# Kernel optimization log

Measured on AMD Instinct MI355X. Metric: run time of the kernel, lower is better.

Reference implementation:

```python
import jax, jax.numpy as jnp
import numpy as np

N = 8192
IN_DIM = 512
OUT_DIM = 512


def setup_inputs() -> dict:
    key = jax.random.key(0)
    kA, kX, k1, k2, k3, k4 = jax.random.split(key, 6)
    A = jax.random.uniform(kA, (N, N), dtype=jnp.float32)  # strictly positive -> nonzero triu
    X = jax.random.normal(kX, (N, IN_DIM), dtype=jnp.float32)
    s = 1.0 / np.sqrt(IN_DIM)
    W1 = jax.random.uniform(k1, (OUT_DIM, IN_DIM), minval=-s, maxval=s, dtype=jnp.float32)  # fc
    b1 = jax.random.uniform(k2, (OUT_DIM,), minval=-s, maxval=s, dtype=jnp.float32)
    W2 = jax.random.uniform(k3, (OUT_DIM, IN_DIM), minval=-s, maxval=s, dtype=jnp.float32)  # fc2
    b2 = jax.random.uniform(k4, (OUT_DIM,), minval=-s, maxval=s, dtype=jnp.float32)
    return {"A": A, "X": X, "W1": W1, "b1": b1, "W2": W2, "b2": b2}


def reference(A, X, W1, b1, W2, b2):
    n = A.shape[0]
    # strictly upper-triangular mask (diagonal=1); with uniform(0,1) fill all these
    # entries are nonzero, so torch.nonzero selects exactly them: m = n(n-1)/2 values.
    triu_mask = jnp.triu(jnp.ones((n, n), dtype=bool), k=1)
    m = n * (n - 1) // 2
    # torch.median = lower median = sorted[(m-1)//2]; pad non-triu entries with +inf
    vals = jnp.where(triu_mask, A, jnp.inf).reshape(-1)
    median_value = jnp.sort(vals)[(m - 1) // 2]
    # A[A < median] = 0
    A_thr = jnp.where(A < median_value, jnp.zeros((), A.dtype), A)
    A_norm = jax.nn.softmax(A_thr, axis=-1)
    fcX = X @ W1.T + b1    # [N, out_dim]
    fc2X = X @ W2.T + b2   # [N, out_dim]
    out = jax.nn.leaky_relu(0.1 * fc2X + 0.9 * (A_norm @ fcX), negative_slope=0.01)
    return out
```

## Files before the change

### kernel.cpp

```cpp
#include <hip/hip_runtime.h>

#define DEVI __device__ __forceinline__

typedef __attribute__((ext_vector_type(8))) short short8;
typedef __attribute__((ext_vector_type(4))) float f32x4;

static constexpr int NN = 8192;
static constexpr int DD = 512;
static constexpr unsigned LOB = 0x3EFE0000u;
static constexpr unsigned HIB = 0x3F020000u;
static constexpr long long K_RANK = 16775167LL;

static constexpr size_t WS_HIST = 0;
static constexpr size_t WS_CNT  = 1048576;
static constexpr size_t WS_MED  = 1048832;
static constexpr size_t WS_XB   = 2097152;
static constexpr size_t WS_W1B  = WS_XB  + (size_t)NN * DD * 2;
static constexpr size_t WS_W2B  = WS_W1B + (size_t)DD * DD * 2;
static constexpr size_t WS_FCXT = WS_W2B + (size_t)DD * DD * 2;
static constexpr size_t WS_FC2  = WS_FCXT + (size_t)NN * DD * 2;
static constexpr size_t WS_UP   = WS_FC2 + (size_t)NN * DD * 4;
static constexpr size_t WS_ZP   = WS_UP  + (size_t)4 * NN * DD * 2;

DEVI unsigned short f2bf(float f) {
  unsigned u = __float_as_uint(f);
  u += 0x7fffu + ((u >> 16) & 1u);
  return (unsigned short)(u >> 16);
}
DEVI float bf2f(unsigned short h) { return __uint_as_float(((unsigned)h) << 16); }
DEVI int swz(int row, int kq) { return kq ^ ((row >> 1) & 3); }

DEVI void gl_lds16(const void* g, void* l) {
  __builtin_amdgcn_global_load_lds(
      (const __attribute__((address_space(1))) unsigned*)g,
      (__attribute__((address_space(3))) unsigned*)l, 16, 0, 0);
}

#define VMCNT(n) asm volatile("s_waitcnt vmcnt(" #n ")" ::: "memory")
#define LGKM0 asm volatile("s_waitcnt lgkmcnt(0)" ::: "memory")

__global__ __launch_bounds__(256) void hist_k(const float* __restrict__ A,
                                              unsigned* __restrict__ hist,
                                              unsigned* __restrict__ below) {
  unsigned cnt = 0;
  const long long nt = (long long)gridDim.x * blockDim.x;
  const float4* A4 = (const float4*)A;
  for (long long q = (long long)blockIdx.x * blockDim.x + threadIdx.x; q < 16777216LL; q += nt) {
    long long base = q << 2;
    int row = (int)(base >> 13);
    int col = (int)(base & 8191);
    if (col + 3 <= row) continue;
    float4 v = A4[q];
    float vv[4] = {v.x, v.y, v.z, v.w};
#pragma unroll
    for (int j = 0; j < 4; ++j) {
      if (col + j > row) {
        unsigned u = __float_as_uint(vv[j]);
        if (u < LOB) cnt++;
        else if (u < HIB) atomicAdd(&hist[u - LOB], 1u);
      }
    }
  }
  for (int off = 32; off > 0; off >>= 1) cnt += __shfl_down(cnt, off);
  if ((threadIdx.x & 63) == 0 && cnt) atomicAdd(below, cnt);
}

__global__ __launch_bounds__(1024) void select_k(const unsigned* __restrict__ hist,
                                                 const unsigned* __restrict__ below,
                                                 unsigned* __restrict__ med) {
  __shared__ unsigned ssum[1024];
  __shared__ int owner;
  __shared__ unsigned tg_s;
  const int t = threadIdx.x;
  unsigned own = 0;
#pragma unroll 4
  for (int b = 0; b < 256; ++b) own += hist[t * 256 + b];
  ssum[t] = own;
  __syncthreads();
  for (int off = 1; off < 1024; off <<= 1) {
    unsigned v = (t >= off) ? ssum[t - off] : 0u;
    __syncthreads();
    ssum[t] += v;
    __syncthreads();
  }
  long long target = K_RANK - (long long)(*below);
  unsigned incl = ssum[t];
  unsigned excl = incl - own;
  if (target >= (long long)excl && target < (long long)incl) {
    owner = t;
    tg_s = (unsigned)(target - (long long)excl);
  }
  __syncthreads();
  const int to = owner;
  const unsigned tg = tg_s;
  unsigned v256 = (t < 256) ? hist[to * 256 + t] : 0u;
  __syncthreads();
  if (t < 256) ssum[t] = v256;
  __syncthreads();
  for (int off = 1; off < 256; off <<= 1) {
    unsigned v = (t < 256 && t >= off) ? ssum[t - off] : 0u;
    __syncthreads();
    if (t < 256) ssum[t] += v;
    __syncthreads();
  }
  if (t < 256) {
    unsigned incl2 = ssum[t];
    unsigned excl2 = incl2 - v256;
    if (tg >= excl2 && tg < incl2) *med = LOB + (unsigned)(to * 256 + t);
  }
}

__global__ __launch_bounds__(256) void convert_k(const float* __restrict__ X,
                                                 const float* __restrict__ W1,
                                                 const float* __restrict__ W2,
                                                 unsigned short* __restrict__ Xb,
                                                 unsigned short* __restrict__ W1b,
                                                 unsigned short* __restrict__ W2b) {
  const long long nt = (long long)gridDim.x * blockDim.x;
  const long long NX = (long long)NN * DD;
  const long long NW = (long long)DD * DD;
  for (long long q = (long long)blockIdx.x * blockDim.x + threadIdx.x; q < (NX + 2 * NW) / 4; q += nt) {
    long long e = q << 2;
    const float4* src; unsigned short* dst; long long off;
    if (e < NX)            { src = (const float4*)X;  dst = Xb;  off = e; }
    else if (e < NX + NW)  { src = (const float4*)W1; dst = W1b; off = e - NX; }
    else                   { src = (const float4*)W2; dst = W2b; off = e - NX - NW; }
    float4 v = src[off >> 2];
    ushort4 o;
    o.x = f2bf(v.x); o.y = f2bf(v.y); o.z = f2bf(v.z); o.w = f2bf(v.w);
    *(ushort4*)(dst + off) = o;
  }
}

template <bool BROW, bool OBF>
__global__ __launch_bounds__(512, 2) void gemm_small_k(const unsigned short* __restrict__ Am,
                                                       const unsigned short* __restrict__ Bm,
                                                       const float* __restrict__ bias,
                                                       void* __restrict__ outp, int ldout) {
  __shared__ alignas(16) unsigned short Ap[64 * 32];
  __shared__ alignas(16) unsigned short Bt[256 * 32];
  char* apB = (char*)Ap;
  char* btB = (char*)Bt;
  const int tid = threadIdx.x, lane = tid & 63, w = tid >> 6;
  const int wm = w >> 2, wn = w & 3;
  const int lr = lane & 15, lq = lane >> 4;
  const int m0 = blockIdx.y * 64, n0 = blockIdx.x * 256;
  const int rL = lane >> 2, kq = lane & 3;
  f32x4 acc[2][4];
#pragma unroll
  for (int i = 0; i < 2; ++i)
#pragma unroll
    for (int j = 0; j < 4; ++j) acc[i][j] = (f32x4){0.f, 0.f, 0.f, 0.f};

#pragma unroll 1
  for (int kt = 0; kt < 16; ++kt) {
    const int k0 = kt * 32;
    __syncthreads();
    if (w < 4) {
      int r = w * 16 + rL;
      gl_lds16(Am + ((size_t)(m0 + r) * DD + k0 + swz(r, kq) * 8), apB + w * 1024);
    }
#pragma unroll
    for (int i = 0; i < 2; ++i) {
      int blk = w * 2 + i;
      int r = blk * 16 + rL;
      gl_lds16(Bm + ((size_t)(n0 + r) * DD + k0 + swz(r, kq) * 8), btB + blk * 1024);
    }
    __syncthreads();
    short8 a[2], b[4];
#pragma unroll
    for (int fr = 0; fr < 2; ++fr) {
      int r = wm * 32 + fr * 16 + lr;
      a[fr] = *(const short8*)(apB + r * 64 + swz(r, lq) * 16);
    }
#pragma unroll
    for (int fc = 0; fc < 4; ++fc) {
      int r = wn * 64 + fc * 16 + lr;
      b[fc] = *(const short8*)(btB + r * 64 + swz(r, lq) * 16);
    }
#pragma unroll
    for (int fr = 0; fr < 2; ++fr)
#pragma unroll
      for (int fc = 0; fc < 4; ++fc)
        acc[fr][fc] = __builtin_amdgcn_mfma_f32_16x16x32_bf16(a[fr], b[fc], acc[fr][fc], 0, 0, 0);
  }
#pragma unroll
  for (int fr = 0; fr < 2; ++fr)
#pragma unroll
    for (int fc = 0; fc < 4; ++fc)
#pragma unroll
      for (int j = 0; j < 4; ++j) {
        int row = m0 + wm * 32 + fr * 16 + lq * 4 + j;
        int col = n0 + wn * 64 + fc * 16 + lr;
        float v = acc[fr][fc][j] + (BROW ? bias[row] : bias[col]);
        if (OBF) ((unsigned short*)outp)[(size_t)row * ldout + col] = f2bf(v);
        else     ((float*)outp)[(size_t)row * ldout + col] = v;
      }
}

static constexpr int LDS_A0 = 0;
static constexpr int LDS_A1 = 8192;
static constexpr int LDS_B0 = 16384;
static constexpr int LDS_B1 = 49152;

__global__ __launch_bounds__(512, 2) void main_gemm_k(const float* __restrict__ A,
                                                      const unsigned short* __restrict__ fcXT,
                                                      const unsigned* __restrict__ medp,
                                                      unsigned short* __restrict__ Up,
                                                      float* __restrict__ Zp) {
  __shared__ alignas(16) char lds[81920];
  const int tid = threadIdx.x, lane = tid & 63, w = tid >> 6;
  const int wm = w >> 2, wn = w & 3;
  const int lr = lane & 15, lq = lane >> 4;
  const int ks = blockIdx.x;
  const int m0 = blockIdx.y * 128;
  const int kbase = ks * 2048;
  const float med = __uint_as_float(*medp);
  const int rB = lane >> 2, kqB = lane & 3;
  const int rA = tid >> 2, cqA = tid & 3;
  const float* aRow = A + (size_t)(m0 + rA) * NN;
  const int ldsAw = rA * 64 + swz(rA, cqA) * 16;

  float zacc = 0.f;
  f32x4 acc[4][8];
#pragma unroll
  for (int i = 0; i < 4; ++i)
#pragma unroll
    for (int j = 0; j < 8; ++j) acc[i][j] = (f32x4){0.f, 0.f, 0.f, 0.f};
  float4 vA00, vA01, vA10, vA11;

#define CONV8(V0, V1, DST)                                                     \
  {                                                                            \
    float vv[8] = {V0.x, V0.y, V0.z, V0.w, V1.x, V1.y, V1.z, V1.w};            \
    short8 pb;                                                                 \
    _Pragma("unroll")                                                          \
    for (int j = 0; j < 8; ++j) {                                              \
      float a_ = vv[j];                                                        \
      float p_ = (a_ < med) ? 1.0f : __expf(a_);                               \
      unsigned short h_ = f2bf(p_);                                            \
      pb[j] = (short)h_;                                                       \
      zacc += bf2f(h_);                                                        \
    }                                                                          \
    *(short8*)(DST) = pb;                                                      \
  }

  {
#pragma unroll
    for (int i = 0; i < 4; ++i) {
      int blk = w * 4 + i;
      int o = blk * 16 + rB;
      gl_lds16(fcXT + ((size_t)o * NN + kbase + swz(o, kqB) * 8), lds + LDS_B0 + blk * 1024);
    }
    const float* ap0 = aRow + kbase + cqA * 8;
    float4 t0 = *(const float4*)ap0;
    float4 t1 = *(const float4*)(ap0 + 4);
    vA00 = *(const float4*)(ap0 + 32);
    vA01 = *(const float4*)(ap0 + 36);
    CONV8(t0, t1, lds + LDS_A0 + ldsAw);
  }
  __syncthreads();

#define ITER(KT, CUR, NCUR, VAC0, VAC1, VAN0, VAN1)                            \
  {                                                                            \
    const int kt_ = (KT);                                                      \
    if (kt_ < 63) {                                                            \
      const int k1 = kbase + (kt_ + 1) * 32;                                   \
      _Pragma("unroll")                                                        \
      for (int i = 0; i < 4; ++i) {                                            \
        int blk = w * 4 + i;                                                   \
        int o = blk * 16 + rB;                                                 \
        gl_lds16(fcXT + ((size_t)o * NN + k1 + swz(o, kqB) * 8),               \
                 lds + LDS_B##NCUR + blk * 1024);                              \
      }                                                                        \
      if (kt_ < 62) {                                                          \
        const float* apf = aRow + kbase + (kt_ + 2) * 32 + cqA * 8;            \
        asm volatile("global_load_dwordx4 %0, %2, off\n\t"                     \
                     "global_load_dwordx4 %1, %2, off offset:16"               \
                     : "=&v"(VAN0), "=&v"(VAN1)                                \
                     : "v"(apf)                                                \
                     : "memory");                                              \
      }                                                                        \
    }                                                                          \
    short8 af[4], bfr[8];                                                      \
    _Pragma("unroll")                                                          \
    for (int fr = 0; fr < 4; ++fr) {                                           \
      int r = wm * 64 + fr * 16 + lr;                                          \
      af[fr] = *(const short8*)(lds + LDS_A##CUR + r * 64 + swz(r, lq) * 16);  \
    }                                                                          \
    _Pragma("unroll")                                                          \
    for (int fc = 0; fc < 8; ++fc) {                                           \
      int o = wn * 128 + fc * 16 + lr;                                         \
      bfr[fc] = *(const short8*)(lds + LDS_B##CUR + o * 64 + swz(o, lq) * 16); \
    }                                                                          \
    __builtin_amdgcn_s_setprio(1);                                             \
    _Pragma("unroll")                                                          \
    for (int fr = 0; fr < 4; ++fr)                                             \
      _Pragma("unroll")                                                        \
      for (int fc = 0; fc < 8; ++fc)                                           \
        acc[fr][fc] = __builtin_amdgcn_mfma_f32_16x16x32_bf16(af[fr], bfr[fc], \
                                                              acc[fr][fc], 0, 0, 0); \
    __builtin_amdgcn_s_setprio(0);                                             \
    if (kt_ < 63) {                                                            \
      if (kt_ < 62) { VMCNT(6); } else { VMCNT(4); }                           \
      __builtin_amdgcn_sched_barrier(0);                                       \
      CONV8(VAC0, VAC1, lds + LDS_A##NCUR + ldsAw);                            \
      if (kt_ < 62) { VMCNT(2); } else { VMCNT(0); }                           \
      LGKM0;                                                                   \
      __builtin_amdgcn_s_barrier();                                            \
    }                                                                          \
  }

#pragma unroll 1
  for (int t2 = 0; t2 < 32; ++t2) {
    ITER(2 * t2,     0, 1, vA00, vA01, vA10, vA11);
    ITER(2 * t2 + 1, 1, 0, vA10, vA11, vA00, vA01);
  }
#undef ITER
#undef CONV8

  zacc += __shfl_xor(zacc, 1);
  zacc += __shfl_xor(zacc, 2);
  if ((lane & 3) == 0) Zp[(size_t)ks * NN + m0 + rA] = zacc;
#pragma unroll
  for (int fr = 0; fr < 4; ++fr)
#pragma unroll
    for (int fc = 0; fc < 8; ++fc)
#pragma unroll
      for (int j = 0; j < 4; ++j) {
        int row = m0 + wm * 64 + fr * 16 + lq * 4 + j;
        int col = wn * 128 + fc * 16 + lr;
        Up[((size_t)ks << 22) + ((size_t)row << 9) + col] = f2bf(acc[fr][fc][j]);
      }
}

__global__ __launch_bounds__(256) void reduce_k(const unsigned short* __restrict__ Up,
                                                const float* __restrict__ Zp,
                                                const float* __restrict__ fc2,
                                                float* __restrict__ out) {
  long long t = (long long)blockIdx.x * blockDim.x + threadIdx.x;
  if (t >= (long long)NN * DD / 8) return;
  long long base = t << 3;
  int row = (int)(base >> 9);
  float Z = Zp[row] + Zp[NN + row] + Zp[2 * NN + row] + Zp[3 * NN + row];
  float inv = 0.9f / Z;
  float s[8] = {0, 0, 0, 0, 0, 0, 0, 0};
#pragma unroll
  for (int sp = 0; sp < 4; ++sp) {
    const uint4 u = *(const uint4*)(Up + ((long long)sp << 22) + base);
    const unsigned uu[4] = {u.x, u.y, u.z, u.w};
#pragma unroll
    for (int j = 0; j < 4; ++j) {
      s[2 * j]     += __uint_as_float(uu[j] << 16);
      s[2 * j + 1] += __uint_as_float(uu[j] & 0xffff0000u);
    }
  }
  float4 fa = *(const float4*)(fc2 + base);
  float4 fb = *(const float4*)(fc2 + base + 4);
  float fv[8] = {fa.x, fa.y, fa.z, fa.w, fb.x, fb.y, fb.z, fb.w};
  float o[8];
#pragma unroll
  for (int j = 0; j < 8; ++j) {
    float v = 0.1f * fv[j] + inv * s[j];
    o[j] = v >= 0.f ? v : 0.01f * v;
  }
  *(float4*)(out + base)     = (float4){o[0], o[1], o[2], o[3]};
  *(float4*)(out + base + 4) = (float4){o[4], o[5], o[6], o[7]};
}

extern "C" void kernel_launch(void* const* d_in, const int* in_sizes, int n_in,
                              void* d_out, int out_size, void* d_ws, size_t ws_size,
                              hipStream_t stream) {
  const float* A  = (const float*)d_in[0];
  const float* X  = (const float*)d_in[1];
  const float* W1 = (const float*)d_in[2];
  const float* b1 = (const float*)d_in[3];
  const float* W2 = (const float*)d_in[4];
  const float* b2 = (const float*)d_in[5];
  char* ws = (char*)d_ws;
  unsigned* hist = (unsigned*)(ws + WS_HIST);
  unsigned* cnt  = (unsigned*)(ws + WS_CNT);
  unsigned* med  = (unsigned*)(ws + WS_MED);
  unsigned short* Xb   = (unsigned short*)(ws + WS_XB);
  unsigned short* W1b  = (unsigned short*)(ws + WS_W1B);
  unsigned short* W2b  = (unsigned short*)(ws + WS_W2B);
  unsigned short* fcXT = (unsigned short*)(ws + WS_FCXT);
  float* fc2           = (float*)(ws + WS_FC2);
  unsigned short* Upp  = (unsigned short*)(ws + WS_UP);
  float* Zp            = (float*)(ws + WS_ZP);

  hipMemsetAsync(ws, 0, 1048576 + 512, stream);
  hipLaunchKernelGGL(hist_k, dim3(2048), dim3(256), 0, stream, A, hist, cnt);
  hipLaunchKernelGGL(select_k, dim3(1), dim3(1024), 0, stream, hist, cnt, med);
  hipLaunchKernelGGL(convert_k, dim3(1024), dim3(256), 0, stream, X, W1, W2, Xb, W1b, W2b);
  hipLaunchKernelGGL((gemm_small_k<true, true>), dim3(32, 8), dim3(512), 0, stream,
                     W1b, Xb, b1, (void*)fcXT, NN);
  hipLaunchKernelGGL((gemm_small_k<false, false>), dim3(2, 128), dim3(512), 0, stream,
                     Xb, W2b, b2, (void*)fc2, DD);
  hipLaunchKernelGGL(main_gemm_k, dim3(4, 64), dim3(512), 0, stream, A, fcXT, med, Upp, Zp);
  hipLaunchKernelGGL(reduce_k, dim3(2048), dim3(256), 0, stream, Upp, Zp, fc2, (float*)d_out);
}
```

Before: 293.6 us.

## Merge hist/convert and both small GEMMs into combined launches, remap grid for XCD locality

Combines the histogram pass and the bf16 conversion into one kernel that splits its blocks by role. It also merges the two small GEMMs into one launch and vectorises the histogram prefix read in select_k. The main GEMM grid becomes 1D, with a block-id mapping that keeps each K-split on a pair of XCDs so those blocks share A rows and fcXT in the same L2. The aim is to cut launch gaps and tail idling between small kernels and to improve cache locality. The cost is role-branching blocks with uneven work in each fused launch.

```diff
diff --git a/kernel.cpp b/kernel.cpp
--- a/kernel.cpp
+++ b/kernel.cpp
@@ -39,13 +39,32 @@
 #define VMCNT(n) asm volatile("s_waitcnt vmcnt(" #n ")" ::: "memory")
 #define LGKM0 asm volatile("s_waitcnt lgkmcnt(0)" ::: "memory")
 
-__global__ __launch_bounds__(256) void hist_k(const float* __restrict__ A,
-                                              unsigned* __restrict__ hist,
-                                              unsigned* __restrict__ below) {
+
+DEVI void convert_body(const float* __restrict__ X, const float* __restrict__ W1,
+                       const float* __restrict__ W2, unsigned short* __restrict__ Xb,
+                       unsigned short* __restrict__ W1b, unsigned short* __restrict__ W2b,
+                       int cb, int tid) {
+  const long long NX = (long long)NN * DD;
+  const long long NW = (long long)DD * DD;
+  const long long total4 = (NX + 2 * NW) / 4;
+  for (long long q = (long long)cb * 512 + tid; q < total4; q += 65536LL) {
+    long long e = q << 2;
+    const float4* src; unsigned short* dst; long long off;
+    if (e < NX)           { src = (const float4*)X;  dst = Xb;  off = e; }
+    else if (e < NX + NW) { src = (const float4*)W1; dst = W1b; off = e - NX; }
+    else                  { src = (const float4*)W2; dst = W2b; off = e - NX - NW; }
+    float4 v = src[off >> 2];
+    ushort4 o;
+    o.x = f2bf(v.x); o.y = f2bf(v.y); o.z = f2bf(v.z); o.w = f2bf(v.w);
+    *(ushort4*)(dst + off) = o;
+  }
+}
+
+DEVI void hist_body(const float* __restrict__ A, unsigned* __restrict__ hist,
+                    unsigned* __restrict__ below, int hb, int tid) {
   unsigned cnt = 0;
-  const long long nt = (long long)gridDim.x * blockDim.x;
   const float4* A4 = (const float4*)A;
-  for (long long q = (long long)blockIdx.x * blockDim.x + threadIdx.x; q < 16777216LL; q += nt) {
+  for (long long q = (long long)hb * 512 + tid; q < 16777216LL; q += 458752LL) {
     long long base = q << 2;
     int row = (int)(base >> 13);
     int col = (int)(base & 8191);
@@ -62,7 +81,103 @@
     }
   }
   for (int off = 32; off > 0; off >>= 1) cnt += __shfl_down(cnt, off);
-  if ((threadIdx.x & 63) == 0 && cnt) atomicAdd(below, cnt);
+  if ((tid & 63) == 0 && cnt) atomicAdd(below, cnt);
+}
+
+__global__ __launch_bounds__(512) void stage1_k(const float* __restrict__ A,
+                                                const float* __restrict__ X,
+                                                const float* __restrict__ W1,
+                                                const float* __restrict__ W2,
+                                                unsigned* __restrict__ hist,
+                                                unsigned* __restrict__ below,
+                                                unsigned short* __restrict__ Xb,
+                                                unsigned short* __restrict__ W1b,
+                                                unsigned short* __restrict__ W2b) {
+  const int bx = blockIdx.x;
+  if (bx < 128) convert_body(X, W1, W2, Xb, W1b, W2b, bx, threadIdx.x);
+  else          hist_body(A, hist, below, bx - 128, threadIdx.x);
+}
+
+
+template <bool BROW, bool OBF>
+DEVI void gemm_small_body(const unsigned short* __restrict__ Am,
+                          const unsigned short* __restrict__ Bm,
+                          const float* __restrict__ bias, void* __restrict__ outp,
+                          int ldout, int m0, int n0, char* apB, char* btB) {
+  const int tid = threadIdx.x, lane = tid & 63, w = tid >> 6;
+  const int wm = w >> 2, wn = w & 3;
+  const int lr = lane & 15, lq = lane >> 4;
+  const int rL = lane >> 2, kq = lane & 3;
+  f32x4 acc[2][4];
+#pragma unroll
+  for (int i = 0; i < 2; ++i)
+#pragma unroll
+    for (int j = 0; j < 4; ++j) acc[i][j] = (f32x4){0.f, 0.f, 0.f, 0.f};
+
+#pragma unroll 1
+  for (int kt = 0; kt < 16; ++kt) {
+    const int k0 = kt * 32;
+    __syncthreads();
+    if (w < 4) {
+      int r = w * 16 + rL;
+      gl_lds16(Am + ((size_t)(m0 + r) * DD + k0 + swz(r, kq) * 8), apB + w * 1024);
+    }
+#pragma unroll
+    for (int i = 0; i < 2; ++i) {
+      int blk = w * 2 + i;
+      int r = blk * 16 + rL;
+      gl_lds16(Bm + ((size_t)(n0 + r) * DD + k0 + swz(r, kq) * 8), btB + blk * 1024);
+    }
+    __syncthreads();
+    short8 a[2], b[4];
+#pragma unroll
+    for (int fr = 0; fr < 2; ++fr) {
+      int r = wm * 32 + fr * 16 + lr;
+      a[fr] = *(const short8*)(apB + r * 64 + swz(r, lq) * 16);
+    }
+#pragma unroll
+    for (int fc = 0; fc < 4; ++fc) {
+      int r = wn * 64 + fc * 16 + lr;
+      b[fc] = *(const short8*)(btB + r * 64 + swz(r, lq) * 16);
+    }
+#pragma unroll
+    for (int fr = 0; fr < 2; ++fr)
+#pragma unroll
+      for (int fc = 0; fc < 4; ++fc)
+        acc[fr][fc] = __builtin_amdgcn_mfma_f32_16x16x32_bf16(a[fr], b[fc], acc[fr][fc], 0, 0, 0);
+  }
+#pragma unroll
+  for (int fr = 0; fr < 2; ++fr)
+#pragma unroll
+    for (int fc = 0; fc < 4; ++fc)
+#pragma unroll
+      for (int j = 0; j < 4; ++j) {
+        int row = m0 + wm * 32 + fr * 16 + lq * 4 + j;
+        int col = n0 + wn * 64 + fc * 16 + lr;
+        float v = acc[fr][fc][j] + (BROW ? bias[row] : bias[col]);
+        if (OBF) ((unsigned short*)outp)[(size_t)row * ldout + col] = f2bf(v);
+        else     ((float*)outp)[(size_t)row * ldout + col] = v;
+      }
+}
+
+__global__ __launch_bounds__(512, 2) void stage2_k(const unsigned short* __restrict__ Xb,
+                                                   const unsigned short* __restrict__ W1b,
+                                                   const unsigned short* __restrict__ W2b,
+                                                   const float* __restrict__ b1,
+                                                   const float* __restrict__ b2,
+                                                   unsigned short* __restrict__ fcXT,
+                                                   float* __restrict__ fc2) {
+  __shared__ alignas(16) char plds[20480];
+  const int bx = blockIdx.x;
+  if (bx < 256) {
+    int m0 = ((bx >> 3) & 7) * 64;
+    int n0 = ((bx & 7) | ((bx >> 6) << 3)) * 256;
+    gemm_small_body<true, true>(W1b, Xb, b1, (void*)fcXT, NN, m0, n0, plds, plds + 4096);
+  } else {
+    int q = bx - 256;
+    gemm_small_body<false, false>(Xb, W2b, b2, (void*)fc2, DD,
+                                  (q >> 1) * 64, (q & 1) * 256, plds, plds + 4096);
+  }
 }
 
 __global__ __launch_bounds__(1024) void select_k(const unsigned* __restrict__ hist,
@@ -73,8 +188,12 @@
   __shared__ unsigned tg_s;
   const int t = threadIdx.x;
   unsigned own = 0;
-#pragma unroll 4
-  for (int b = 0; b < 256; ++b) own += hist[t * 256 + b];
+  const uint4* h4 = (const uint4*)(hist + t * 256);
+#pragma unroll 8
+  for (int b = 0; b < 64; ++b) {
+    uint4 v = h4[b];
+    own += v.x + v.y + v.z + v.w;
+  }
   ssum[t] = own;
   __syncthreads();
   for (int off = 1; off < 1024; off <<= 1) {
@@ -110,94 +229,6 @@
   }
 }
 
-__global__ __launch_bounds__(256) void convert_k(const float* __restrict__ X,
-                                                 const float* __restrict__ W1,
-                                                 const float* __restrict__ W2,
-                                                 unsigned short* __restrict__ Xb,
-                                                 unsigned short* __restrict__ W1b,
-                                                 unsigned short* __restrict__ W2b) {
-  const long long nt = (long long)gridDim.x * blockDim.x;
-  const long long NX = (long long)NN * DD;
-  const long long NW = (long long)DD * DD;
-  for (long long q = (long long)blockIdx.x * blockDim.x + threadIdx.x; q < (NX + 2 * NW) / 4; q += nt) {
-    long long e = q << 2;
-    const float4* src; unsigned short* dst; long long off;
-    if (e < NX)            { src = (const float4*)X;  dst = Xb;  off = e; }
-    else if (e < NX + NW)  { src = (const float4*)W1; dst = W1b; off = e - NX; }
-    else                   { src = (const float4*)W2; dst = W2b; off = e - NX - NW; }
-    float4 v = src[off >> 2];
-    ushort4 o;
-    o.x = f2bf(v.x); o.y = f2bf(v.y); o.z = f2bf(v.z); o.w = f2bf(v.w);
-    *(ushort4*)(dst + off) = o;
-  }
-}
-
-template <bool BROW, bool OBF>
-__global__ __launch_bounds__(512, 2) void gemm_small_k(const unsigned short* __restrict__ Am,
-                                                       const unsigned short* __restrict__ Bm,
-                                                       const float* __restrict__ bias,
-                                                       void* __restrict__ outp, int ldout) {
-  __shared__ alignas(16) unsigned short Ap[64 * 32];
-  __shared__ alignas(16) unsigned short Bt[256 * 32];
-  char* apB = (char*)Ap;
-  char* btB = (char*)Bt;
-  const int tid = threadIdx.x, lane = tid & 63, w = tid >> 6;
-  const int wm = w >> 2, wn = w & 3;
-  const int lr = lane & 15, lq = lane >> 4;
-  const int m0 = blockIdx.y * 64, n0 = blockIdx.x * 256;
-  const int rL = lane >> 2, kq = lane & 3;
-  f32x4 acc[2][4];
-#pragma unroll
-  for (int i = 0; i < 2; ++i)
-#pragma unroll
-    for (int j = 0; j < 4; ++j) acc[i][j] = (f32x4){0.f, 0.f, 0.f, 0.f};
-
-#pragma unroll 1
-  for (int kt = 0; kt < 16; ++kt) {
-    const int k0 = kt * 32;
-    __syncthreads();
-    if (w < 4) {
-      int r = w * 16 + rL;
-      gl_lds16(Am + ((size_t)(m0 + r) * DD + k0 + swz(r, kq) * 8), apB + w * 1024);
-    }
-#pragma unroll
-    for (int i = 0; i < 2; ++i) {
-      int blk = w * 2 + i;
-      int r = blk * 16 + rL;
-      gl_lds16(Bm + ((size_t)(n0 + r) * DD + k0 + swz(r, kq) * 8), btB + blk * 1024);
-    }
-    __syncthreads();
-    short8 a[2], b[4];
-#pragma unroll
-    for (int fr = 0; fr < 2; ++fr) {
-      int r = wm * 32 + fr * 16 + lr;
-      a[fr] = *(const short8*)(apB + r * 64 + swz(r, lq) * 16);
-    }
-#pragma unroll
-    for (int fc = 0; fc < 4; ++fc) {
-      int r = wn * 64 + fc * 16 + lr;
-      b[fc] = *(const short8*)(btB + r * 64 + swz(r, lq) * 16);
-    }
-#pragma unroll
-    for (int fr = 0; fr < 2; ++fr)
-#pragma unroll
-      for (int fc = 0; fc < 4; ++fc)
-        acc[fr][fc] = __builtin_amdgcn_mfma_f32_16x16x32_bf16(a[fr], b[fc], acc[fr][fc], 0, 0, 0);
-  }
-#pragma unroll
-  for (int fr = 0; fr < 2; ++fr)
-#pragma unroll
-    for (int fc = 0; fc < 4; ++fc)
-#pragma unroll
-      for (int j = 0; j < 4; ++j) {
-        int row = m0 + wm * 32 + fr * 16 + lq * 4 + j;
-        int col = n0 + wn * 64 + fc * 16 + lr;
-        float v = acc[fr][fc][j] + (BROW ? bias[row] : bias[col]);
-        if (OBF) ((unsigned short*)outp)[(size_t)row * ldout + col] = f2bf(v);
-        else     ((float*)outp)[(size_t)row * ldout + col] = v;
-      }
-}
-
 static constexpr int LDS_A0 = 0;
 static constexpr int LDS_A1 = 8192;
 static constexpr int LDS_B0 = 16384;
@@ -212,8 +243,10 @@
   const int tid = threadIdx.x, lane = tid & 63, w = tid >> 6;
   const int wm = w >> 2, wn = w & 3;
   const int lr = lane & 15, lq = lane >> 4;
-  const int ks = blockIdx.x;
-  const int m0 = blockIdx.y * 128;
+  const int fid = blockIdx.x;
+  const int xcd = fid & 7;
+  const int ks = xcd >> 1;
+  const int m0 = (((xcd & 1) << 5) | (fid >> 3)) << 7;
   const int kbase = ks * 2048;
   const float med = __uint_as_float(*medp);
   const int rB = lane >> 2, kqB = lane & 3;
@@ -389,13 +422,11 @@
   float* Zp            = (float*)(ws + WS_ZP);
 
   hipMemsetAsync(ws, 0, 1048576 + 512, stream);
-  hipLaunchKernelGGL(hist_k, dim3(2048), dim3(256), 0, stream, A, hist, cnt);
+  hipLaunchKernelGGL(stage1_k, dim3(1024), dim3(512), 0, stream,
+                     A, X, W1, W2, hist, cnt, Xb, W1b, W2b);
+  hipLaunchKernelGGL(stage2_k, dim3(512), dim3(512), 0, stream,
+                     Xb, W1b, W2b, b1, b2, fcXT, fc2);
   hipLaunchKernelGGL(select_k, dim3(1), dim3(1024), 0, stream, hist, cnt, med);
-  hipLaunchKernelGGL(convert_k, dim3(1024), dim3(256), 0, stream, X, W1, W2, Xb, W1b, W2b);
-  hipLaunchKernelGGL((gemm_small_k<true, true>), dim3(32, 8), dim3(512), 0, stream,
-                     W1b, Xb, b1, (void*)fcXT, NN);
-  hipLaunchKernelGGL((gemm_small_k<false, false>), dim3(2, 128), dim3(512), 0, stream,
-                     Xb, W2b, b2, (void*)fc2, DD);
-  hipLaunchKernelGGL(main_gemm_k, dim3(4, 64), dim3(512), 0, stream, A, fcXT, med, Upp, Zp);
+  hipLaunchKernelGGL(main_gemm_k, dim3(256), dim3(512), 0, stream, A, fcXT, med, Upp, Zp);
   hipLaunchKernelGGL(reduce_k, dim3(2048), dim3(256), 0, stream, Upp, Zp, fc2, (float*)d_out);
 }
```

After: 268.4 us. -8.6%, faster.
